# Optimization experiments

Measured on AMD Instinct MI355X. Metric: run time of the kernel, lower is better.

Reference implementation:

```python
import jax, jax.numpy as jnp
import numpy as np

B, T = 16384, 128  # batch, n_frames


def setup_inputs() -> dict:
    key = jax.random.key(0)
    k0, k1, k2, k3, k4, k5 = jax.random.split(key, 6)
    dir = jax.random.normal(k0, (B, 3), dtype=jnp.float32)
    R = jax.random.normal(k1, (B, T, 3, 3), dtype=jnp.float32)
    s = 1.0 / np.sqrt(3.0)  # torch LSTM default init scale (uniform +-1/sqrt(hidden))
    W_ih = jax.random.uniform(k2, (12, 3), jnp.float32, -s, s)
    W_hh = jax.random.uniform(k3, (12, 3), jnp.float32, -s, s)
    b_ih = jax.random.uniform(k4, (12,), jnp.float32, -s, s)
    b_hh = jax.random.uniform(k5, (12,), jnp.float32, -s, s)
    return {"dir": dir, "R": R, "W_ih": W_ih, "W_hh": W_hh, "b_ih": b_ih, "b_hh": b_hh}


def _rot_step(v, Rm):
    # v: [B,3], Rm: [B,3,3] -> Rm @ v
    nv = jnp.einsum('bij,bj->bi', Rm, v)
    return nv, nv


def _build_dirs(dir, R):
    n_frames = R.shape[1]
    half = n_frames // 2
    # Backward chain: dirs[i] = R[half-1-i]^T @ ... @ R[half-1]^T @ dir
    Rt_back = jnp.swapaxes(jnp.flip(R[:, :half], axis=1), 2, 3)  # [B, half, 3, 3]
    _, back = jax.lax.scan(_rot_step, dir, jnp.swapaxes(Rt_back, 0, 1))  # [half, B, 3]
    # Forward chain: dirs[i] = R[i-1] @ ... @ R[half] @ dir for i in half+1..n-1
    Rf = jnp.swapaxes(R[:, half:n_frames - 1], 0, 1)  # [n-1-half, B, 3, 3]
    _, fwd = jax.lax.scan(_rot_step, dir, Rf)  # [n-1-half, B, 3]
    dirs_tm = jnp.concatenate([back, dir[None], fwd], axis=0)  # time-major [T, B, 3]
    return dirs_tm, half


def _lstm(dirs_tm, W_ih, W_hh, b_ih, b_hh):
    Bsz = dirs_tm.shape[1]
    h0 = jnp.zeros((Bsz, 3), dirs_tm.dtype)
    c0 = jnp.zeros((Bsz, 3), dirs_tm.dtype)
    bias = b_ih + b_hh

    def step(carry, x):
        h, c = carry
        gates = x @ W_ih.T + h @ W_hh.T + bias  # [B,12]
        i = jax.nn.sigmoid(gates[:, 0:3])
        f = jax.nn.sigmoid(gates[:, 3:6])
        g = jnp.tanh(gates[:, 6:9])
        o = jax.nn.sigmoid(gates[:, 9:12])
        c = f * c + i * g
        h = o * jnp.tanh(c)
        return (h, c), h

    _, h_seq = jax.lax.scan(step, (h0, c0), dirs_tm)  # [T, B, 3]
    return h_seq


def reference(dir, R, W_ih, W_hh, b_ih, b_hh):
    dirs_tm, half = _build_dirs(dir, R)
    h_seq = _lstm(dirs_tm, W_ih, W_hh, b_ih, b_hh)
    dirs_out = jnp.swapaxes(dirs_tm, 0, 1)  # [B, T, 3]
    return dirs_out.at[:, half, :].set(h_seq[half])
```

## Files before the change

### kernel.cpp

```cpp
#include <hip/hip_runtime.h>

typedef float f4 __attribute__((ext_vector_type(4)));
typedef float f4u __attribute__((ext_vector_type(4), aligned(4)));

struct M3 { float m[3][3]; };

#define ELEM(q, n) ((q)[(n) >> 2][(n) & 3])

__device__ __forceinline__ M3 matmul(const M3& A, const M3& B) {
  M3 C;
#pragma unroll
  for (int i = 0; i < 3; ++i)
#pragma unroll
    for (int j = 0; j < 3; ++j)
      C.m[i][j] = A.m[i][0]*B.m[0][j] + A.m[i][1]*B.m[1][j] + A.m[i][2]*B.m[2][j];
  return C;
}

__device__ __forceinline__ M3 mk18(const f4 (&q)[18], int k) {
  M3 A;
#pragma unroll
  for (int i = 0; i < 3; ++i)
#pragma unroll
    for (int j = 0; j < 3; ++j)
      A.m[i][j] = ELEM(q, 9*k + 3*i + j);
  return A;
}

template <int CTRL>
__device__ __forceinline__ float dppf(float v) {
  return __int_as_float(
      __builtin_amdgcn_mov_dpp(__float_as_int(v), CTRL, 0xf, 0xf, true));
}

template <int D>
__device__ __forceinline__ M3 dpp_shr_mat(const M3& A) {
  M3 C;
#pragma unroll
  for (int i = 0; i < 3; ++i)
#pragma unroll
    for (int j = 0; j < 3; ++j)
      C.m[i][j] = dppf<0x110 + D>(A.m[i][j]);
  return C;
}

__device__ __forceinline__ float sigm(float z) {
  return __builtin_amdgcn_rcpf(1.0f + __expf(-z));
}
__device__ __forceinline__ float tanh_(float z) {
  float e = __expf(2.0f * z);
  return 1.0f - 2.0f * __builtin_amdgcn_rcpf(e + 1.0f);
}

template <int CTRL>
__device__ __forceinline__ float quad_bcast(float v) {
  return __int_as_float(
      __builtin_amdgcn_mov_dpp(__float_as_int(v), CTRL, 0xf, 0xf, true));
}

__global__ __launch_bounds__(64) void fused_kernel(
    const float* __restrict__ dir, const float* __restrict__ R,
    const float* __restrict__ Wih, const float* __restrict__ Whh,
    const float* __restrict__ bih, const float* __restrict__ bhh,
    float* __restrict__ out, int B) {
  __shared__ __align__(16) f4 xrows[64 * 16];

  const int lane = threadIdx.x;
  const int e8 = lane >> 3;
  const int s = lane & 7;
  const int b0 = blockIdx.x * 16;

  f4 qN[18];
  {
    int bn = b0 + e8; bn = (bn < B) ? bn : (B - 1);
    const f4* p = (const f4*)(R + (size_t)bn * 1152) + 18 * (7 - s);
#pragma unroll
    for (int i = 0; i < 18; ++i) qN[i] = p[i];
  }

#pragma unroll 1
  for (int it = 0; it < 4; ++it) {
    const int g = it >> 1;
    const int phase = it & 1;
    const int b = b0 + g * 8 + e8;
    const bool valid = (b < B);
    const int bc = valid ? b : (B - 1);

    f4 q[18];
#pragma unroll
    for (int i = 0; i < 18; ++i) q[i] = qN[i];

    if (it < 3) {
      const int itn = it + 1;
      int bn = b0 + (itn >> 1) * 8 + e8; bn = (bn < B) ? bn : (B - 1);
      const f4* p = (const f4*)(R + (size_t)bn * 1152) +
                    ((itn & 1) ? (144 + 18 * s) : (18 * (7 - s)));
#pragma unroll
      for (int i = 0; i < 18; ++i) qN[i] = p[i];
    }

    const float d0 = dir[3*bc+0], d1 = dir[3*bc+1], d2 = dir[3*bc+2];

    M3 P = mk18(q, 0);
#pragma unroll
    for (int k = 1; k < 8; ++k) P = matmul(mk18(q, k), P);

    M3 I = P;
    {
      M3 Sh = dpp_shr_mat<1>(I);
      M3 T; if (phase == 0) T = matmul(Sh, I); else T = matmul(I, Sh);
#pragma unroll
      for (int i = 0; i < 3; ++i)
#pragma unroll
        for (int j = 0; j < 3; ++j) I.m[i][j] = (s >= 1) ? T.m[i][j] : I.m[i][j];
    }
    {
      M3 Sh = dpp_shr_mat<2>(I);
      M3 T; if (phase == 0) T = matmul(Sh, I); else T = matmul(I, Sh);
#pragma unroll
      for (int i = 0; i < 3; ++i)
#pragma unroll
        for (int j = 0; j < 3; ++j) I.m[i][j] = (s >= 2) ? T.m[i][j] : I.m[i][j];
    }
    {
      M3 Sh = dpp_shr_mat<4>(I);
      M3 T; if (phase == 0) T = matmul(Sh, I); else T = matmul(I, Sh);
#pragma unroll
      for (int i = 0; i < 3; ++i)
#pragma unroll
        for (int j = 0; j < 3; ++j) I.m[i][j] = (s >= 4) ? T.m[i][j] : I.m[i][j];
    }

    if (phase == 0) {
      float w0 = I.m[0][0]*d0 + I.m[1][0]*d1 + I.m[2][0]*d2;
      float w1 = I.m[0][1]*d0 + I.m[1][1]*d1 + I.m[2][1]*d2;
      float w2 = I.m[0][2]*d0 + I.m[1][2]*d1 + I.m[2][2]*d2;
      float p0 = dppf<0x111>(w0), p1 = dppf<0x111>(w1), p2 = dppf<0x111>(w2);
      float v0 = (s == 0) ? d0 : p0;
      float v1 = (s == 0) ? d1 : p1;
      float v2 = (s == 0) ? d2 : p2;

      float row[24];
#pragma unroll
      for (int j = 0; j < 8; ++j) {
        M3 A = mk18(q, 7 - j);
        float n0 = v0*A.m[0][0] + v1*A.m[1][0] + v2*A.m[2][0];
        float n1 = v0*A.m[0][1] + v1*A.m[1][1] + v2*A.m[2][1];
        float n2 = v0*A.m[0][2] + v1*A.m[1][2] + v2*A.m[2][2];
        v0 = n0; v1 = n1; v2 = n2;
        row[3*j+0] = n0; row[3*j+1] = n1; row[3*j+2] = n2;
      }

      if (valid) {
        float* ob = out + (size_t)b * 384 + 24 * s;
#pragma unroll
        for (int kk = 0; kk < 6; ++kk) {
          f4 vv = { row[4*kk+0], row[4*kk+1], row[4*kk+2], row[4*kk+3] };
          ((f4*)ob)[kk] = vv;
        }
      }
#pragma unroll
      for (int j = 0; j < 8; ++j) {
        f4 vv = { row[3*j+0], row[3*j+1], row[3*j+2], 0.f };
        xrows[(8*s + j) * 16 + g * 8 + e8] = vv;
      }
    } else {
      float w0 = I.m[0][0]*d0 + I.m[0][1]*d1 + I.m[0][2]*d2;
      float w1 = I.m[1][0]*d0 + I.m[1][1]*d1 + I.m[1][2]*d2;
      float w2 = I.m[2][0]*d0 + I.m[2][1]*d1 + I.m[2][2]*d2;
      float p0 = dppf<0x111>(w0), p1 = dppf<0x111>(w1), p2 = dppf<0x111>(w2);
      float v0 = (s == 0) ? d0 : p0;
      float v1 = (s == 0) ? d1 : p1;
      float v2 = (s == 0) ? d2 : p2;

      float row[24];
#pragma unroll
      for (int j = 0; j < 8; ++j) {
        M3 A = mk18(q, j);
        float n0 = A.m[0][0]*v0 + A.m[0][1]*v1 + A.m[0][2]*v2;
        float n1 = A.m[1][0]*v0 + A.m[1][1]*v1 + A.m[1][2]*v2;
        float n2 = A.m[2][0]*v0 + A.m[2][1]*v1 + A.m[2][2]*v2;
        v0 = n0; v1 = n1; v2 = n2;
        row[3*j+0] = n0; row[3*j+1] = n1; row[3*j+2] = n2;
      }

      if (valid) {
        float* ob = out + (size_t)b * 384 + (size_t)(65 + 8*s) * 3;
#pragma unroll
        for (int kk = 0; kk < 5; ++kk) {
          f4u vv = { row[4*kk+0], row[4*kk+1], row[4*kk+2], row[4*kk+3] };
          *(f4u*)(ob + 4*kk) = vv;
        }
        ob[20] = row[20];
        if (s < 7) { ob[21] = row[21]; ob[22] = row[22]; ob[23] = row[23]; }
      }
    }
  }

  const int e2 = lane >> 2;
  const int u = lane & 3, uu = (u == 3) ? 0 : u;
  const int b2 = b0 + e2;
  const bool valid2 = (b2 < B);
  const int b2c = valid2 ? b2 : 0;

  const float wii0 = Wih[uu*3+0],     wii1 = Wih[uu*3+1],     wii2 = Wih[uu*3+2];
  const float wif0 = Wih[(3+uu)*3+0], wif1 = Wih[(3+uu)*3+1], wif2 = Wih[(3+uu)*3+2];
  const float wig0 = Wih[(6+uu)*3+0], wig1 = Wih[(6+uu)*3+1], wig2 = Wih[(6+uu)*3+2];
  const float wio0 = Wih[(9+uu)*3+0], wio1 = Wih[(9+uu)*3+1], wio2 = Wih[(9+uu)*3+2];
  const float whi0 = Whh[uu*3+0],     whi1 = Whh[uu*3+1],     whi2 = Whh[uu*3+2];
  const float whf0 = Whh[(3+uu)*3+0], whf1 = Whh[(3+uu)*3+1], whf2 = Whh[(3+uu)*3+2];
  const float whg0 = Whh[(6+uu)*3+0], whg1 = Whh[(6+uu)*3+1], whg2 = Whh[(6+uu)*3+2];
  const float who0 = Whh[(9+uu)*3+0], who1 = Whh[(9+uu)*3+1], who2 = Whh[(9+uu)*3+2];
  const float bsi = bih[uu]   + bhh[uu];
  const float bsf = bih[3+uu] + bhh[3+uu];
  const float bsg = bih[6+uu] + bhh[6+uu];
  const float bso = bih[9+uu] + bhh[9+uu];
  const float dd0 = dir[3*b2c+0], dd1 = dir[3*b2c+1], dd2 = dir[3*b2c+2];

  float h0 = 0.f, h1 = 0.f, h2 = 0.f, cc = 0.f, hl = 0.f;

#define LSTEP(x0_, x1_, x2_)                                                  \
  {                                                                           \
    float zi = bsi + wii0*(x0_) + wii1*(x1_) + wii2*(x2_)                     \
                   + whi0*h0 + whi1*h1 + whi2*h2;                             \
    float zf = bsf + wif0*(x0_) + wif1*(x1_) + wif2*(x2_)                     \
                   + whf0*h0 + whf1*h1 + whf2*h2;                             \
    float zg = bsg + wig0*(x0_) + wig1*(x1_) + wig2*(x2_)                     \
                   + whg0*h0 + whg1*h1 + whg2*h2;                             \
    float zo = bso + wio0*(x0_) + wio1*(x1_) + wio2*(x2_)                     \
                   + who0*h0 + who1*h1 + who2*h2;                             \
    float ai = sigm(zi), af = sigm(zf), ag = tanh_(zg), ao = sigm(zo);        \
    cc = af*cc + ai*ag;                                                       \
    float hn = ao * tanh_(cc);                                                \
    hl = hn;                                                                  \
    h0 = quad_bcast<0x00>(hn);                                                \
    h1 = quad_bcast<0x55>(hn);                                                \
    h2 = quad_bcast<0xAA>(hn);                                                \
  }

#pragma unroll 1
  for (int c = 0; c < 8; ++c) {
    f4 xa[8];
#pragma unroll
    for (int j = 0; j < 8; ++j) xa[j] = xrows[(c * 8 + j) * 16 + e2];
#pragma unroll
    for (int j = 0; j < 8; ++j) LSTEP(xa[j][0], xa[j][1], xa[j][2]);
  }
  LSTEP(dd0, dd1, dd2);
#undef LSTEP

  if (valid2 && u < 3) out[(size_t)b2 * 384 + 192 + u] = hl;
}

extern "C" void kernel_launch(void* const* d_in, const int* in_sizes, int n_in,
                              void* d_out, int out_size, void* d_ws, size_t ws_size,
                              hipStream_t stream) {
  const float* dir = (const float*)d_in[0];
  const float* R   = (const float*)d_in[1];
  const float* Wih = (const float*)d_in[2];
  const float* Whh = (const float*)d_in[3];
  const float* bih = (const float*)d_in[4];
  const float* bhh = (const float*)d_in[5];
  float* out = (float*)d_out;

  const int B = in_sizes[0] / 3;
  const int grid = (B + 15) / 16;
  hipLaunchKernelGGL(fused_kernel, dim3(grid), dim3(64), 0, stream,
                     dir, R, Wih, Whh, bih, bhh, out, B);
}
```

Measured before the change: 34.38 us.

## Split fused kernel into parallel chain kernel and separate LSTM kernel via workspace

Splits the fused kernel into two launches. The first computes the backward and forward rotation chains, one chain per 8-batch block, which quadruples the grid and removes the serial 4-iteration loop. It writes the backward-chain inputs to a global workspace instead of LDS. The second kernel runs the LSTM recurrence, reading inputs from the workspace with double-buffered prefetch, at the cost of an extra launch and a global round-trip of the intermediate data.

```diff
diff --git a/kernel.cpp b/kernel.cpp
--- a/kernel.cpp
+++ b/kernel.cpp
@@ -58,150 +58,136 @@
       __builtin_amdgcn_mov_dpp(__float_as_int(v), CTRL, 0xf, 0xf, true));
 }
 
-__global__ __launch_bounds__(64) void fused_kernel(
+__global__ __launch_bounds__(64) void chains_kernel(
     const float* __restrict__ dir, const float* __restrict__ R,
-    const float* __restrict__ Wih, const float* __restrict__ Whh,
-    const float* __restrict__ bih, const float* __restrict__ bhh,
-    float* __restrict__ out, int B) {
-  __shared__ __align__(16) f4 xrows[64 * 16];
-
+    float* __restrict__ out, f4* __restrict__ ws, int B, int nbBack) {
   const int lane = threadIdx.x;
   const int e8 = lane >> 3;
   const int s = lane & 7;
-  const int b0 = blockIdx.x * 16;
-
-  f4 qN[18];
-  {
-    int bn = b0 + e8; bn = (bn < B) ? bn : (B - 1);
-    const f4* p = (const f4*)(R + (size_t)bn * 1152) + 18 * (7 - s);
-#pragma unroll
-    for (int i = 0; i < 18; ++i) qN[i] = p[i];
-  }
-
-#pragma unroll 1
-  for (int it = 0; it < 4; ++it) {
-    const int g = it >> 1;
-    const int phase = it & 1;
-    const int b = b0 + g * 8 + e8;
-    const bool valid = (b < B);
-    const int bc = valid ? b : (B - 1);
-
-    f4 q[18];
-#pragma unroll
-    for (int i = 0; i < 18; ++i) q[i] = qN[i];
-
-    if (it < 3) {
-      const int itn = it + 1;
-      int bn = b0 + (itn >> 1) * 8 + e8; bn = (bn < B) ? bn : (B - 1);
-      const f4* p = (const f4*)(R + (size_t)bn * 1152) +
-                    ((itn & 1) ? (144 + 18 * s) : (18 * (7 - s)));
-#pragma unroll
-      for (int i = 0; i < 18; ++i) qN[i] = p[i];
-    }
-
-    const float d0 = dir[3*bc+0], d1 = dir[3*bc+1], d2 = dir[3*bc+2];
-
-    M3 P = mk18(q, 0);
-#pragma unroll
-    for (int k = 1; k < 8; ++k) P = matmul(mk18(q, k), P);
-
-    M3 I = P;
-    {
-      M3 Sh = dpp_shr_mat<1>(I);
-      M3 T; if (phase == 0) T = matmul(Sh, I); else T = matmul(I, Sh);
-#pragma unroll
-      for (int i = 0; i < 3; ++i)
-#pragma unroll
-        for (int j = 0; j < 3; ++j) I.m[i][j] = (s >= 1) ? T.m[i][j] : I.m[i][j];
-    }
-    {
-      M3 Sh = dpp_shr_mat<2>(I);
-      M3 T; if (phase == 0) T = matmul(Sh, I); else T = matmul(I, Sh);
-#pragma unroll
-      for (int i = 0; i < 3; ++i)
-#pragma unroll
-        for (int j = 0; j < 3; ++j) I.m[i][j] = (s >= 2) ? T.m[i][j] : I.m[i][j];
-    }
-    {
-      M3 Sh = dpp_shr_mat<4>(I);
-      M3 T; if (phase == 0) T = matmul(Sh, I); else T = matmul(I, Sh);
-#pragma unroll
-      for (int i = 0; i < 3; ++i)
-#pragma unroll
-        for (int j = 0; j < 3; ++j) I.m[i][j] = (s >= 4) ? T.m[i][j] : I.m[i][j];
-    }
-
-    if (phase == 0) {
-      float w0 = I.m[0][0]*d0 + I.m[1][0]*d1 + I.m[2][0]*d2;
-      float w1 = I.m[0][1]*d0 + I.m[1][1]*d1 + I.m[2][1]*d2;
-      float w2 = I.m[0][2]*d0 + I.m[1][2]*d1 + I.m[2][2]*d2;
-      float p0 = dppf<0x111>(w0), p1 = dppf<0x111>(w1), p2 = dppf<0x111>(w2);
-      float v0 = (s == 0) ? d0 : p0;
-      float v1 = (s == 0) ? d1 : p1;
-      float v2 = (s == 0) ? d2 : p2;
-
-      float row[24];
-#pragma unroll
-      for (int j = 0; j < 8; ++j) {
-        M3 A = mk18(q, 7 - j);
-        float n0 = v0*A.m[0][0] + v1*A.m[1][0] + v2*A.m[2][0];
-        float n1 = v0*A.m[0][1] + v1*A.m[1][1] + v2*A.m[2][1];
-        float n2 = v0*A.m[0][2] + v1*A.m[1][2] + v2*A.m[2][2];
-        v0 = n0; v1 = n1; v2 = n2;
-        row[3*j+0] = n0; row[3*j+1] = n1; row[3*j+2] = n2;
+  const bool isBack = ((int)blockIdx.x < nbBack);
+  const int blk = isBack ? (int)blockIdx.x : ((int)blockIdx.x - nbBack);
+  const int b = blk * 8 + e8;
+  const bool valid = (b < B);
+  const int bc = valid ? b : (B - 1);
+
+  f4 q[18];
+  {
+    const f4* p = (const f4*)(R + (size_t)bc * 1152) +
+                  (isBack ? 18 * (7 - s) : (144 + 18 * s));
+#pragma unroll
+    for (int i = 0; i < 18; ++i) q[i] = p[i];
+  }
+  const float d0 = dir[3*bc+0], d1 = dir[3*bc+1], d2 = dir[3*bc+2];
+
+  M3 P = mk18(q, 0);
+#pragma unroll
+  for (int k = 1; k < 8; ++k) P = matmul(mk18(q, k), P);
+
+  M3 I = P;
+  {
+    M3 Sh = dpp_shr_mat<1>(I);
+    M3 T; if (isBack) T = matmul(Sh, I); else T = matmul(I, Sh);
+#pragma unroll
+    for (int i = 0; i < 3; ++i)
+#pragma unroll
+      for (int j = 0; j < 3; ++j) I.m[i][j] = (s >= 1) ? T.m[i][j] : I.m[i][j];
+  }
+  {
+    M3 Sh = dpp_shr_mat<2>(I);
+    M3 T; if (isBack) T = matmul(Sh, I); else T = matmul(I, Sh);
+#pragma unroll
+    for (int i = 0; i < 3; ++i)
+#pragma unroll
+      for (int j = 0; j < 3; ++j) I.m[i][j] = (s >= 2) ? T.m[i][j] : I.m[i][j];
+  }
+  {
+    M3 Sh = dpp_shr_mat<4>(I);
+    M3 T; if (isBack) T = matmul(Sh, I); else T = matmul(I, Sh);
+#pragma unroll
+    for (int i = 0; i < 3; ++i)
+#pragma unroll
+      for (int j = 0; j < 3; ++j) I.m[i][j] = (s >= 4) ? T.m[i][j] : I.m[i][j];
+  }
+
+  float w0, w1, w2;
+  if (isBack) {
+    w0 = I.m[0][0]*d0 + I.m[1][0]*d1 + I.m[2][0]*d2;
+    w1 = I.m[0][1]*d0 + I.m[1][1]*d1 + I.m[2][1]*d2;
+    w2 = I.m[0][2]*d0 + I.m[1][2]*d1 + I.m[2][2]*d2;
+  } else {
+    w0 = I.m[0][0]*d0 + I.m[0][1]*d1 + I.m[0][2]*d2;
+    w1 = I.m[1][0]*d0 + I.m[1][1]*d1 + I.m[1][2]*d2;
+    w2 = I.m[2][0]*d0 + I.m[2][1]*d1 + I.m[2][2]*d2;
+  }
+  float p0 = dppf<0x111>(w0), p1 = dppf<0x111>(w1), p2 = dppf<0x111>(w2);
+  float v0 = (s == 0) ? d0 : p0;
+  float v1 = (s == 0) ? d1 : p1;
+  float v2 = (s == 0) ? d2 : p2;
+
+  float row[24];
+  if (isBack) {
+#pragma unroll
+    for (int j = 0; j < 8; ++j) {
+      M3 A = mk18(q, 7 - j);
+      float n0 = v0*A.m[0][0] + v1*A.m[1][0] + v2*A.m[2][0];
+      float n1 = v0*A.m[0][1] + v1*A.m[1][1] + v2*A.m[2][1];
+      float n2 = v0*A.m[0][2] + v1*A.m[1][2] + v2*A.m[2][2];
+      v0 = n0; v1 = n1; v2 = n2;
+      row[3*j+0] = n0; row[3*j+1] = n1; row[3*j+2] = n2;
+    }
+  } else {
+#pragma unroll
+    for (int j = 0; j < 8; ++j) {
+      M3 A = mk18(q, j);
+      float n0 = A.m[0][0]*v0 + A.m[0][1]*v1 + A.m[0][2]*v2;
+      float n1 = A.m[1][0]*v0 + A.m[1][1]*v1 + A.m[1][2]*v2;
+      float n2 = A.m[2][0]*v0 + A.m[2][1]*v1 + A.m[2][2]*v2;
+      v0 = n0; v1 = n1; v2 = n2;
+      row[3*j+0] = n0; row[3*j+1] = n1; row[3*j+2] = n2;
+    }
+  }
+
+  if (isBack) {
+    if (valid) {
+      float* ob = out + (size_t)b * 384 + 24 * s;
+#pragma unroll
+      for (int kk = 0; kk < 6; ++kk) {
+        f4 vv = { row[4*kk+0], row[4*kk+1], row[4*kk+2], row[4*kk+3] };
+        ((f4*)ob)[kk] = vv;
       }
-
-      if (valid) {
-        float* ob = out + (size_t)b * 384 + 24 * s;
-#pragma unroll
-        for (int kk = 0; kk < 6; ++kk) {
-          f4 vv = { row[4*kk+0], row[4*kk+1], row[4*kk+2], row[4*kk+3] };
-          ((f4*)ob)[kk] = vv;
-        }
-      }
+      f4* wp = ws + (size_t)b * 64 + 8 * s;
 #pragma unroll
       for (int j = 0; j < 8; ++j) {
         f4 vv = { row[3*j+0], row[3*j+1], row[3*j+2], 0.f };
-        xrows[(8*s + j) * 16 + g * 8 + e8] = vv;
+        wp[j] = vv;
       }
-    } else {
-      float w0 = I.m[0][0]*d0 + I.m[0][1]*d1 + I.m[0][2]*d2;
-      float w1 = I.m[1][0]*d0 + I.m[1][1]*d1 + I.m[1][2]*d2;
-      float w2 = I.m[2][0]*d0 + I.m[2][1]*d1 + I.m[2][2]*d2;
-      float p0 = dppf<0x111>(w0), p1 = dppf<0x111>(w1), p2 = dppf<0x111>(w2);
-      float v0 = (s == 0) ? d0 : p0;
-      float v1 = (s == 0) ? d1 : p1;
-      float v2 = (s == 0) ? d2 : p2;
-
-      float row[24];
-#pragma unroll
-      for (int j = 0; j < 8; ++j) {
-        M3 A = mk18(q, j);
-        float n0 = A.m[0][0]*v0 + A.m[0][1]*v1 + A.m[0][2]*v2;
-        float n1 = A.m[1][0]*v0 + A.m[1][1]*v1 + A.m[1][2]*v2;
-        float n2 = A.m[2][0]*v0 + A.m[2][1]*v1 + A.m[2][2]*v2;
-        v0 = n0; v1 = n1; v2 = n2;
-        row[3*j+0] = n0; row[3*j+1] = n1; row[3*j+2] = n2;
+    }
+  } else {
+    if (valid) {
+      float* ob = out + (size_t)b * 384 + (size_t)(65 + 8*s) * 3;
+#pragma unroll
+      for (int kk = 0; kk < 5; ++kk) {
+        f4u vv = { row[4*kk+0], row[4*kk+1], row[4*kk+2], row[4*kk+3] };
+        *(f4u*)(ob + 4*kk) = vv;
       }
-
-      if (valid) {
-        float* ob = out + (size_t)b * 384 + (size_t)(65 + 8*s) * 3;
-#pragma unroll
-        for (int kk = 0; kk < 5; ++kk) {
-          f4u vv = { row[4*kk+0], row[4*kk+1], row[4*kk+2], row[4*kk+3] };
-          *(f4u*)(ob + 4*kk) = vv;
-        }
-        ob[20] = row[20];
-        if (s < 7) { ob[21] = row[21]; ob[22] = row[22]; ob[23] = row[23]; }
-      }
-    }
-  }
-
+      ob[20] = row[20];
+      if (s < 7) { ob[21] = row[21]; ob[22] = row[22]; ob[23] = row[23]; }
+    }
+  }
+}
+
+__global__ __launch_bounds__(64) void lstm_kernel(
+    const float* __restrict__ dir,
+    const float* __restrict__ Wih, const float* __restrict__ Whh,
+    const float* __restrict__ bih, const float* __restrict__ bhh,
+    float* __restrict__ out, const f4* __restrict__ ws, int B) {
+  const int lane = threadIdx.x;
   const int e2 = lane >> 2;
   const int u = lane & 3, uu = (u == 3) ? 0 : u;
-  const int b2 = b0 + e2;
+  const int b2 = blockIdx.x * 16 + e2;
   const bool valid2 = (b2 < B);
   const int b2c = valid2 ? b2 : 0;
+  const f4* xp = ws + (size_t)b2c * 64;
 
   const float wii0 = Wih[uu*3+0],     wii1 = Wih[uu*3+1],     wii2 = Wih[uu*3+2];
   const float wif0 = Wih[(3+uu)*3+0], wif1 = Wih[(3+uu)*3+1], wif2 = Wih[(3+uu)*3+2];
@@ -238,13 +224,21 @@
     h2 = quad_bcast<0xAA>(hn);                                                \
   }
 
+  f4 xa[8], xb[8];
+#pragma unroll
+  for (int j = 0; j < 8; ++j) xa[j] = xp[j];
 #pragma unroll 1
-  for (int c = 0; c < 8; ++c) {
-    f4 xa[8];
-#pragma unroll
-    for (int j = 0; j < 8; ++j) xa[j] = xrows[(c * 8 + j) * 16 + e2];
+  for (int cp = 0; cp < 4; ++cp) {
+#pragma unroll
+    for (int j = 0; j < 8; ++j) xb[j] = xp[(2*cp + 1) * 8 + j];
 #pragma unroll
     for (int j = 0; j < 8; ++j) LSTEP(xa[j][0], xa[j][1], xa[j][2]);
+    if (cp < 3) {
+#pragma unroll
+      for (int j = 0; j < 8; ++j) xa[j] = xp[(2*cp + 2) * 8 + j];
+    }
+#pragma unroll
+    for (int j = 0; j < 8; ++j) LSTEP(xb[j][0], xb[j][1], xb[j][2]);
   }
   LSTEP(dd0, dd1, dd2);
 #undef LSTEP
@@ -262,9 +256,13 @@
   const float* bih = (const float*)d_in[4];
   const float* bhh = (const float*)d_in[5];
   float* out = (float*)d_out;
+  f4* ws = (f4*)d_ws;
 
   const int B = in_sizes[0] / 3;
-  const int grid = (B + 15) / 16;
-  hipLaunchKernelGGL(fused_kernel, dim3(grid), dim3(64), 0, stream,
-                     dir, R, Wih, Whh, bih, bhh, out, B);
-}
+  const int nbBack = (B + 7) / 8;
+  hipLaunchKernelGGL(chains_kernel, dim3(nbBack * 2), dim3(64), 0, stream,
+                     dir, R, out, ws, B, nbBack);
+  const int gridB = (B + 15) / 16;
+  hipLaunchKernelGGL(lstm_kernel, dim3(gridB), dim3(64), 0, stream,
+                     dir, Wih, Whh, bih, bhh, out, ws, B);
+}
```

After: 50.99 us. 48.3% more time.
